# Kernel optimization log

Measured on AMD Instinct MI355X. Metric: run time of the kernel, lower is better.

The kernel has to match this reference:

```python
import jax, jax.numpy as jnp
import numpy as np

N_NODES = 20000
N_EDGES = 320000
F_IN = 512
F_OUT = 1024
N_GRAPHS = 64


def gcn_conv(x, src, dst, ew, W, b, n_nodes):
    xw = x @ W  # [N, Fout]
    loop = jnp.arange(n_nodes)
    s = jnp.concatenate([src, loop])
    d = jnp.concatenate([dst, loop])
    w = jnp.concatenate([ew, jnp.ones((n_nodes,), dtype=x.dtype)])
    deg = jax.ops.segment_sum(w, d, num_segments=n_nodes)  # in-degree by weight
    dinv = jnp.where(deg > 0, jax.lax.rsqrt(deg), 0.0).astype(x.dtype)
    norm = dinv[s] * w * dinv[d]  # [E+N]
    msg = norm[:, None] * xw[s]  # [E+N, Fout]
    out = jax.ops.segment_sum(msg, d, num_segments=n_nodes)
    return out + b


def mean_pool(x, batch, n_graphs):
    sums = jax.ops.segment_sum(x, batch, num_segments=n_graphs)
    cnt = jax.ops.segment_sum(jnp.ones((x.shape[0],), dtype=x.dtype), batch, num_segments=n_graphs)
    return sums / jnp.maximum(cnt, 1.0)[:, None]


def setup_inputs() -> dict:
    key = jax.random.key(0)
    ks = jax.random.split(key, 8)
    node_features = jax.random.normal(ks[0], (N_NODES, F_IN), dtype=jnp.float32)
    edge_index = jax.random.randint(ks[1], (2, N_EDGES), 0, N_NODES, dtype=jnp.int64)
    edge_weight = jax.random.uniform(ks[2], (N_EDGES,), dtype=jnp.float32)
    batch = jnp.sort(jax.random.randint(ks[3], (N_NODES,), 0, N_GRAPHS, dtype=jnp.int64))
    # Glorot-style params for the two GCNConv layers
    W1 = jax.random.normal(ks[4], (F_IN, F_OUT), dtype=jnp.float32) / np.sqrt(F_IN)
    b1 = jnp.zeros((F_OUT,), dtype=jnp.float32)
    W2 = jax.random.normal(ks[5], (F_OUT, F_OUT), dtype=jnp.float32) / np.sqrt(F_OUT)
    b2 = jnp.zeros((F_OUT,), dtype=jnp.float32)
    return {"node_features": node_features, "edge_index": edge_index,
            "edge_weight": edge_weight, "batch": batch,
            "W1": W1, "b1": b1, "W2": W2, "b2": b2}


def reference(node_features, edge_index, edge_weight, batch, W1, b1, W2, b2):
    n_nodes = node_features.shape[0]
    src, dst = edge_index[0], edge_index[1]
    h = jax.nn.relu(gcn_conv(node_features, src, dst, edge_weight, W1, b1, n_nodes))
    h = jax.nn.relu(gcn_conv(h, src, dst, edge_weight, W2, b2, n_nodes))
    return mean_pool(h, batch, N_GRAPHS)  # [G, F_OUT]
```

## Files before the change

kernel.cpp:

```cpp
#include <hip/hip_runtime.h>

#define N_NODES 20000
#define N_PAD   20480
#define N_EDGES 320000
#define F_IN 512
#define F_OUT 1024
#define N_GRAPHS 64
#define ESTRIDE 64

typedef __attribute__((ext_vector_type(8))) short bf16x8;
typedef __attribute__((ext_vector_type(4))) float f32x4;
typedef __attribute__((ext_vector_type(8))) unsigned short ushort8v;

static __device__ __forceinline__ unsigned short f2bf(float f) {
    unsigned int u = __float_as_uint(f);
    u = (u + 0x7fff + ((u >> 16) & 1)) >> 16;
    return (unsigned short)u;
}
static __device__ __forceinline__ float bf2f(unsigned short s) {
    return __uint_as_float(((unsigned int)s) << 16);
}

__global__ void k_setup(float* deg, int* cursor, float* out,
                        const int* __restrict__ batch, int* gstart) {
    int i = blockIdx.x * 256 + threadIdx.x;
    if (i < N_NODES) { deg[i] = 1.0f; cursor[i] = 0; }
    if (i < N_GRAPHS * F_OUT) out[i] = 0.f;
    if (i <= N_GRAPHS) {
        if (i == N_GRAPHS) gstart[i] = N_NODES;
        else {
            int lo = 0, hi = N_NODES;
            while (lo < hi) {
                int mid = (lo + hi) >> 1;
                if (batch[mid] < i) lo = mid + 1; else hi = mid;
            }
            gstart[i] = lo;
        }
    }
}

#define NB_E    ((N_EDGES + 255) / 256)
#define NB_WT   ((F_OUT / 32) * (F_IN / 32 + F_OUT / 32))
#define NB_CX   (N_PAD * (F_IN / 8) / 256)
__global__ __launch_bounds__(256) void k_pre(const int* __restrict__ dst,
                                             const float* __restrict__ ew,
                                             float* deg,
                                             const float* __restrict__ W1,
                                             unsigned short* __restrict__ Wt1,
                                             const float* __restrict__ W2,
                                             unsigned short* __restrict__ Wt2,
                                             const float* __restrict__ x,
                                             unsigned short* __restrict__ xb) {
    __shared__ float tile[32][33];
    const int bid = blockIdx.x;
    if (bid < NB_E) {
        int e = bid * 256 + threadIdx.x;
        if (e < N_EDGES) atomicAdd(&deg[dst[e]], ew[e]);
    } else if (bid < NB_E + NB_WT) {
        int cid = bid - NB_E;
        int by = cid >> 5;
        int n0 = (cid & 31) * 32;
        const float* W; unsigned short* Wt; int K, k0;
        if (by < F_IN / 32) { W = W1; Wt = Wt1; K = F_IN;  k0 = by * 32; }
        else                { W = W2; Wt = Wt2; K = F_OUT; k0 = (by - F_IN / 32) * 32; }
        int tx = threadIdx.x & 31;
        int ty = threadIdx.x >> 5;
#pragma unroll
        for (int i = 0; i < 32; i += 8)
            tile[ty + i][tx] = W[(size_t)(k0 + ty + i) * F_OUT + n0 + tx];
        __syncthreads();
#pragma unroll
        for (int i = 0; i < 32; i += 8)
            Wt[(size_t)(n0 + ty + i) * K + k0 + tx] = f2bf(tile[tx][ty + i]);
    } else {
        int idx = (bid - NB_E - NB_WT) * 256 + threadIdx.x;
        int row = idx >> 6;
        int c8 = (idx & 63) * 8;
        if (row >= N_PAD) return;
        ushort8v v;
        if (row < N_NODES) {
            const float* p = &x[(size_t)row * F_IN + c8];
#pragma unroll
            for (int i = 0; i < 8; i++) v[i] = f2bf(p[i]);
        } else {
#pragma unroll
            for (int i = 0; i < 8; i++) v[i] = 0;
        }
        *(ushort8v*)&xb[(size_t)row * F_IN + c8] = v;
    }
}

__global__ void k_fill(const int* __restrict__ src, const int* __restrict__ dst,
                       const float* __restrict__ ew, const float* __restrict__ deg,
                       int* cursor, unsigned int* __restrict__ csre) {
    int e = blockIdx.x * 256 + threadIdx.x;
    if (e < N_EDGES) {
        int d = dst[e], s = src[e];
        int pos = atomicAdd(&cursor[d], 1);
        if (pos < ESTRIDE) {
            float w = rsqrtf(deg[s]) * ew[e] * rsqrtf(deg[d]);
            csre[d * ESTRIDE + pos] = ((unsigned int)f2bf(w) << 16) | (unsigned int)s;
        }
    }
}

__global__ __launch_bounds__(64) void k_aggr_slab(const unsigned short* __restrict__ xin,
                                                  const float* __restrict__ deg,
                                                  const int* __restrict__ cursor,
                                                  const unsigned int* __restrict__ csre,
                                                  const float* __restrict__ bias,
                                                  unsigned short* __restrict__ outp,
                                                  int F, int act) {
    const int bid = blockIdx.x;
    const int slab = bid & 7;
    const int ng = bid >> 3;
    const int lane = threadIdx.x;
    const int n = ng * 8 + (lane >> 3);
    const int c = blockIdx.y * 512 + slab * 64 + (lane & 7) * 8;

    if (n >= N_NODES) {
        ushort8v z;
#pragma unroll
        for (int i = 0; i < 8; i++) z[i] = 0;
        *(ushort8v*)&outp[(size_t)n * F + c] = z;
        return;
    }

    const float di = rsqrtf(deg[n]);
    const float wself = di * di;
    float a[8];
    {
        ushort8v v = *(const ushort8v*)&xin[(size_t)n * F + c];
#pragma unroll
        for (int i = 0; i < 8; i++) a[i] = bf2f(v[i]) * wself;
    }

    const unsigned int* ce = csre + (size_t)n * ESTRIDE;
    const int cnt = min(cursor[n], ESTRIDE);
    int j = 0;
    for (; j + 4 <= cnt; j += 4) {
        uint4 m = *(const uint4*)&ce[j];
        ushort8v u0 = *(const ushort8v*)&xin[(size_t)(m.x & 0xFFFF) * F + c];
        ushort8v u1 = *(const ushort8v*)&xin[(size_t)(m.y & 0xFFFF) * F + c];
        ushort8v u2 = *(const ushort8v*)&xin[(size_t)(m.z & 0xFFFF) * F + c];
        ushort8v u3 = *(const ushort8v*)&xin[(size_t)(m.w & 0xFFFF) * F + c];
        float w0 = bf2f((unsigned short)(m.x >> 16));
        float w1 = bf2f((unsigned short)(m.y >> 16));
        float w2 = bf2f((unsigned short)(m.z >> 16));
        float w3 = bf2f((unsigned short)(m.w >> 16));
#pragma unroll
        for (int i = 0; i < 8; i++) {
            a[i] += w0 * bf2f(u0[i]);
            a[i] += w1 * bf2f(u1[i]);
            a[i] += w2 * bf2f(u2[i]);
            a[i] += w3 * bf2f(u3[i]);
        }
    }
    for (; j < cnt; j++) {
        unsigned int m = ce[j];
        float w = bf2f((unsigned short)(m >> 16));
        ushort8v u = *(const ushort8v*)&xin[(size_t)(m & 0xFFFF) * F + c];
#pragma unroll
        for (int i = 0; i < 8; i++) a[i] += w * bf2f(u[i]);
    }

    ushort8v r;
    if (act) {
#pragma unroll
        for (int i = 0; i < 8; i++) r[i] = f2bf(fmaxf(a[i] + bias[c + i], 0.f));
    } else {
#pragma unroll
        for (int i = 0; i < 8; i++) r[i] = f2bf(a[i]);
    }
    *(ushort8v*)&outp[(size_t)n * F + c] = r;
}

__global__ __launch_bounds__(512) void k_gemm_ring3(const unsigned short* __restrict__ A,
                                                    const unsigned short* __restrict__ Bt,
                                                    unsigned short* __restrict__ C, int K,
                                                    const float* __restrict__ bias, int act) {
    __shared__ short As[3][128 * 64];
    __shared__ short Bs[3][256 * 64];

    const int bid = blockIdx.x;
    const int xcd = bid & 7;
    const int i2 = bid >> 3;
    const int colb = i2 & 3;
    const int rowb = xcd * 20 + (i2 >> 2);
    const int row0 = rowb * 128;
    const int col0 = colb * 256;

    const int tid = threadIdx.x;
    const int lane = tid & 63;
    const int wave = tid >> 6;
    const int wm = wave >> 2;
    const int wn = wave & 3;
    const int l16 = lane & 15;
    const int kq = lane >> 4;

    const int NT = K >> 6;

    f32x4 acc[4][4] = {};

    auto stage = [&](int t, int s) {
        const int k0 = t * 64;
#pragma unroll
        for (int it = 0; it < 2; it++) {
            int q = it * 512 + tid;
            int r = q >> 3;
            int g = (q & 7) ^ (r & 7);
            __builtin_amdgcn_global_load_lds(
                (const __attribute__((address_space(1))) void*)&A[(size_t)(row0 + r) * K + k0 + g * 8],
                (__attribute__((address_space(3))) void*)&As[s][q * 8], 16, 0, 0);
        }
#pragma unroll
        for (int it = 0; it < 4; it++) {
            int q = it * 512 + tid;
            int r = q >> 3;
            int g = (q & 7) ^ (r & 7);
            __builtin_amdgcn_global_load_lds(
                (const __attribute__((address_space(1))) void*)&Bt[(size_t)(col0 + r) * K + k0 + g * 8],
                (__attribute__((address_space(3))) void*)&Bs[s][q * 8], 16, 0, 0);
        }
    };

    stage(0, 0);
    stage(1, 1);
    asm volatile("s_waitcnt vmcnt(6)" ::: "memory");
    __builtin_amdgcn_s_barrier();
    __builtin_amdgcn_sched_barrier(0);

    int s = 0;
    for (int t = 0; t < NT; ++t) {
        int s2 = s + 2; if (s2 >= 3) s2 -= 3;
        if (t + 2 < NT) stage(t + 2, s2);

        const short* Asl = As[s];
        const short* Bsl = Bs[s];
#pragma unroll
        for (int ks = 0; ks < 2; ks++) {
            bf16x8 af[4], bfr[4];
#pragma unroll
            for (int fr = 0; fr < 4; fr++) {
                int r = wm * 64 + fr * 16 + l16;
                int g = (ks * 4 + kq) ^ (r & 7);
                af[fr] = *(const bf16x8*)&Asl[r * 64 + g * 8];
            }
#pragma unroll
            for (int fc = 0; fc < 4; fc++) {
                int r = wn * 64 + fc * 16 + l16;
                int g = (ks * 4 + kq) ^ (r & 7);
                bfr[fc] = *(const bf16x8*)&Bsl[r * 64 + g * 8];
            }
            __builtin_amdgcn_s_setprio(1);
#pragma unroll
            for (int fr = 0; fr < 4; fr++)
#pragma unroll
                for (int fc = 0; fc < 4; fc++)
                    acc[fr][fc] = __builtin_amdgcn_mfma_f32_16x16x32_bf16(
                        af[fr], bfr[fc], acc[fr][fc], 0, 0, 0);
            __builtin_amdgcn_s_setprio(0);
        }

        if (t < NT - 1) {
            if (t + 2 < NT) asm volatile("s_waitcnt vmcnt(6)" ::: "memory");
            else            asm volatile("s_waitcnt vmcnt(0)" ::: "memory");
            __builtin_amdgcn_s_barrier();
            __builtin_amdgcn_sched_barrier(0);
        }
        s = s + 1; if (s >= 3) s -= 3;
    }

#pragma unroll
    for (int fr = 0; fr < 4; fr++) {
        int m0 = row0 + wm * 64 + fr * 16 + kq * 4;
#pragma unroll
        for (int fc = 0; fc < 4; fc++) {
            int n = col0 + wn * 64 + fc * 16 + l16;
            float bv = act ? bias[n] : 0.f;
#pragma unroll
            for (int reg = 0; reg < 4; reg++) {
                float v = acc[fr][fc][reg];
                if (act) v = fmaxf(v + bv, 0.f);
                C[(size_t)(m0 + reg) * F_OUT + n] = f2bf(v);
            }
        }
    }
}

__global__ __launch_bounds__(256) void k_pool(const unsigned short* __restrict__ h,
                                              const int* __restrict__ batch,
                                              const int* __restrict__ gstart,
                                              float* __restrict__ out) {
    const int r0 = blockIdx.x * 64;
    const int rowsub = threadIdx.x >> 7;
    const int c = (threadIdx.x & 127) * 8;
    const int rend = min(r0 + 64, N_NODES);
    int row = r0 + rowsub;
    if (row >= rend) return;

    float a[8] = {};
    int gcur = batch[row];
    for (; row < rend; row += 2) {
        int g = batch[row];
        if (g != gcur) {
            float inv = 1.0f / (float)max(gstart[gcur + 1] - gstart[gcur], 1);
#pragma unroll
            for (int i = 0; i < 8; i++) {
                atomicAdd(&out[(size_t)gcur * F_OUT + c + i], a[i] * inv);
                a[i] = 0.f;
            }
            gcur = g;
        }
        ushort8v v = *(const ushort8v*)&h[(size_t)row * F_OUT + c];
#pragma unroll
        for (int i = 0; i < 8; i++) a[i] += bf2f(v[i]);
    }
    float inv = 1.0f / (float)max(gstart[gcur + 1] - gstart[gcur], 1);
#pragma unroll
    for (int i = 0; i < 8; i++)
        atomicAdd(&out[(size_t)gcur * F_OUT + c + i], a[i] * inv);
}

extern "C" void kernel_launch(void* const* d_in, const int* in_sizes, int n_in,
                              void* d_out, int out_size, void* d_ws, size_t ws_size,
                              hipStream_t stream) {
    const float* x    = (const float*)d_in[0];
    const int* ei     = (const int*)d_in[1];
    const float* ew   = (const float*)d_in[2];
    const int* batch  = (const int*)d_in[3];
    const float* W1   = (const float*)d_in[4];
    const float* b1   = (const float*)d_in[5];
    const float* W2   = (const float*)d_in[6];
    const float* b2   = (const float*)d_in[7];
    float* out = (float*)d_out;

    const int* src = ei;
    const int* dst = ei + N_EDGES;

    char* ws = (char*)d_ws;
    const size_t SZ_XB  = (size_t)N_PAD * F_IN * 2;
    const size_t SZ_AX  = (size_t)N_PAD * F_IN * 2;
    const size_t SZ_WT1 = (size_t)F_OUT * F_IN * 2;
    const size_t SZ_WT2 = (size_t)F_OUT * F_OUT * 2;
    const size_t SZ_B   = (size_t)N_PAD * F_OUT * 2;
    unsigned short* xb  = (unsigned short*)(ws);
    unsigned short* ax  = (unsigned short*)(ws + SZ_XB);
    unsigned short* Wt1 = (unsigned short*)(ws + SZ_XB + SZ_AX);
    unsigned short* Wt2 = (unsigned short*)(ws + SZ_XB + SZ_AX + SZ_WT1);
    unsigned short* h1  = (unsigned short*)(ws + SZ_XB + SZ_AX + SZ_WT1 + SZ_WT2);
    unsigned short* xw2 = (unsigned short*)(ws + SZ_XB + SZ_AX + SZ_WT1 + SZ_WT2 + SZ_B);
    unsigned short* h2  = (unsigned short*)(ws);
    size_t off = SZ_XB + SZ_AX + SZ_WT1 + SZ_WT2 + 2 * SZ_B;
    auto alloc = [&](size_t bytes) -> void* {
        void* p = ws + off;
        off += (bytes + 255) & ~(size_t)255;
        return p;
    };
    float*        deg    = (float*)       alloc((size_t)N_NODES * 4);
    int*          cursor = (int*)         alloc((size_t)N_NODES * 4);
    unsigned int* csre   = (unsigned int*)alloc((size_t)N_NODES * ESTRIDE * 4);
    int*          gstart = (int*)         alloc((size_t)(N_GRAPHS + 1) * 4);

    k_setup<<<(N_GRAPHS * F_OUT + 255) / 256, 256, 0, stream>>>(deg, cursor, out, batch, gstart);
    k_pre<<<NB_E + NB_WT + NB_CX, 256, 0, stream>>>(dst, ew, deg, W1, Wt1, W2, Wt2, x, xb);
    k_fill<<<NB_E, 256, 0, stream>>>(src, dst, ew, deg, cursor, csre);
    k_aggr_slab<<<dim3((N_PAD / 8) * 8, 1), 64, 0, stream>>>(xb, deg, cursor, csre,
                                                             (const float*)nullptr, ax, F_IN, 0);
    const int gemm_blocks = (N_PAD / 128) * (F_OUT / 256);
    k_gemm_ring3<<<gemm_blocks, 512, 0, stream>>>(ax, Wt1, h1, F_IN, b1, 1);
    k_gemm_ring3<<<gemm_blocks, 512, 0, stream>>>(h1, Wt2, xw2, F_OUT, (const float*)nullptr, 0);
    k_aggr_slab<<<dim3((N_PAD / 8) * 8, 2), 64, 0, stream>>>(xw2, deg, cursor, csre, b2, h2, F_OUT, 1);
    k_pool<<<(N_NODES + 63) / 64, 256, 0, stream>>>(h2, batch, gstart, out);
}
```

Baseline: 375.0 us.

## Fuse mean-pool into second aggregation and switch GEMM to double-buffered 128x128 tiles

```diff
diff --git a/kernel.cpp b/kernel.cpp
--- a/kernel.cpp
+++ b/kernel.cpp
@@ -110,7 +110,10 @@
                                                   const unsigned int* __restrict__ csre,
                                                   const float* __restrict__ bias,
                                                   unsigned short* __restrict__ outp,
-                                                  int F, int act) {
+                                                  int F, int act,
+                                                  const int* __restrict__ batch,
+                                                  const int* __restrict__ gstart,
+                                                  float* __restrict__ pool_out) {
     const int bid = blockIdx.x;
     const int slab = bid & 7;
     const int ng = bid >> 3;
@@ -119,10 +122,12 @@
     const int c = blockIdx.y * 512 + slab * 64 + (lane & 7) * 8;
 
     if (n >= N_NODES) {
-        ushort8v z;
-#pragma unroll
-        for (int i = 0; i < 8; i++) z[i] = 0;
-        *(ushort8v*)&outp[(size_t)n * F + c] = z;
+        if (!pool_out) {
+            ushort8v z;
+#pragma unroll
+            for (int i = 0; i < 8; i++) z[i] = 0;
+            *(ushort8v*)&outp[(size_t)n * F + c] = z;
+        }
         return;
     }
 
@@ -164,6 +169,33 @@
         for (int i = 0; i < 8; i++) a[i] += w * bf2f(u[i]);
     }
 
+    if (pool_out) {
+        float v[8];
+#pragma unroll
+        for (int i = 0; i < 8; i++) v[i] = fmaxf(a[i] + bias[c + i], 0.f);
+        const int g0 = batch[ng * 8];
+        const int g7 = batch[ng * 8 + 7];
+        if (g0 == g7) {
+            const float inv = 1.0f / (float)max(gstart[g0 + 1] - gstart[g0], 1);
+#pragma unroll
+            for (int m = 8; m < 64; m <<= 1)
+#pragma unroll
+                for (int i = 0; i < 8; i++) v[i] += __shfl_xor(v[i], m, 64);
+            if ((lane >> 3) == 0) {
+#pragma unroll
+                for (int i = 0; i < 8; i++)
+                    atomicAdd(&pool_out[(size_t)g0 * F_OUT + c + i], v[i] * inv);
+            }
+        } else {
+            const int g = batch[n];
+            const float inv = 1.0f / (float)max(gstart[g + 1] - gstart[g], 1);
+#pragma unroll
+            for (int i = 0; i < 8; i++)
+                atomicAdd(&pool_out[(size_t)g * F_OUT + c + i], v[i] * inv);
+        }
+        return;
+    }
+
     ushort8v r;
     if (act) {
 #pragma unroll
@@ -175,49 +207,40 @@
     *(ushort8v*)&outp[(size_t)n * F + c] = r;
 }
 
-__global__ __launch_bounds__(512) void k_gemm_ring3(const unsigned short* __restrict__ A,
-                                                    const unsigned short* __restrict__ Bt,
-                                                    unsigned short* __restrict__ C, int K,
-                                                    const float* __restrict__ bias, int act) {
-    __shared__ short As[3][128 * 64];
-    __shared__ short Bs[3][256 * 64];
-
+__global__ __launch_bounds__(256) void k_gemm_db(const unsigned short* __restrict__ A,
+                                                 const unsigned short* __restrict__ Bt,
+                                                 unsigned short* __restrict__ C, int K,
+                                                 const float* __restrict__ bias, int act) {
+    __shared__ short As[2][128 * 64];
+    __shared__ short Bs[2][128 * 64];
     const int bid = blockIdx.x;
     const int xcd = bid & 7;
     const int i2 = bid >> 3;
-    const int colb = i2 & 3;
-    const int rowb = xcd * 20 + (i2 >> 2);
+    const int colb = i2 & 7;
+    const int rowb = xcd * 20 + (i2 >> 3);
     const int row0 = rowb * 128;
-    const int col0 = colb * 256;
+    const int col0 = colb * 128;
 
     const int tid = threadIdx.x;
     const int lane = tid & 63;
     const int wave = tid >> 6;
-    const int wm = wave >> 2;
-    const int wn = wave & 3;
+    const int wm = wave >> 1, wn = wave & 1;
     const int l16 = lane & 15;
     const int kq = lane >> 4;
 
     const int NT = K >> 6;
-
     f32x4 acc[4][4] = {};
 
     auto stage = [&](int t, int s) {
         const int k0 = t * 64;
 #pragma unroll
-        for (int it = 0; it < 2; it++) {
-            int q = it * 512 + tid;
+        for (int it = 0; it < 4; it++) {
+            int q = it * 256 + tid;
             int r = q >> 3;
             int g = (q & 7) ^ (r & 7);
             __builtin_amdgcn_global_load_lds(
                 (const __attribute__((address_space(1))) void*)&A[(size_t)(row0 + r) * K + k0 + g * 8],
                 (__attribute__((address_space(3))) void*)&As[s][q * 8], 16, 0, 0);
-        }
-#pragma unroll
-        for (int it = 0; it < 4; it++) {
-            int q = it * 512 + tid;
-            int r = q >> 3;
-            int g = (q & 7) ^ (r & 7);
             __builtin_amdgcn_global_load_lds(
                 (const __attribute__((address_space(1))) void*)&Bt[(size_t)(col0 + r) * K + k0 + g * 8],
                 (__attribute__((address_space(3))) void*)&Bs[s][q * 8], 16, 0, 0);
@@ -225,16 +248,14 @@
     };
 
     stage(0, 0);
-    stage(1, 1);
-    asm volatile("s_waitcnt vmcnt(6)" ::: "memory");
-    __builtin_amdgcn_s_barrier();
-    __builtin_amdgcn_sched_barrier(0);
+    __syncthreads();
 
     int s = 0;
     for (int t = 0; t < NT; ++t) {
-        int s2 = s + 2; if (s2 >= 3) s2 -= 3;
-        if (t + 2 < NT) stage(t + 2, s2);
-
+        if (t + 1 < NT) {
+            stage(t + 1, s ^ 1);
+            __builtin_amdgcn_sched_barrier(0);
+        }
         const short* Asl = As[s];
         const short* Bsl = Bs[s];
 #pragma unroll
@@ -261,14 +282,10 @@
                         af[fr], bfr[fc], acc[fr][fc], 0, 0, 0);
             __builtin_amdgcn_s_setprio(0);
         }
-
-        if (t < NT - 1) {
-            if (t + 2 < NT) asm volatile("s_waitcnt vmcnt(6)" ::: "memory");
-            else            asm volatile("s_waitcnt vmcnt(0)" ::: "memory");
-            __builtin_amdgcn_s_barrier();
-            __builtin_amdgcn_sched_barrier(0);
-        }
-        s = s + 1; if (s >= 3) s -= 3;
+        if (t + 1 < NT) {
+            __syncthreads();
+            s ^= 1;
+        }
     }
 
 #pragma unroll
@@ -286,40 +303,6 @@
             }
         }
     }
-}
-
-__global__ __launch_bounds__(256) void k_pool(const unsigned short* __restrict__ h,
-                                              const int* __restrict__ batch,
-                                              const int* __restrict__ gstart,
-                                              float* __restrict__ out) {
-    const int r0 = blockIdx.x * 64;
-    const int rowsub = threadIdx.x >> 7;
-    const int c = (threadIdx.x & 127) * 8;
-    const int rend = min(r0 + 64, N_NODES);
-    int row = r0 + rowsub;
-    if (row >= rend) return;
-
-    float a[8] = {};
-    int gcur = batch[row];
-    for (; row < rend; row += 2) {
-        int g = batch[row];
-        if (g != gcur) {
-            float inv = 1.0f / (float)max(gstart[gcur + 1] - gstart[gcur], 1);
-#pragma unroll
-            for (int i = 0; i < 8; i++) {
-                atomicAdd(&out[(size_t)gcur * F_OUT + c + i], a[i] * inv);
-                a[i] = 0.f;
-            }
-            gcur = g;
-        }
-        ushort8v v = *(const ushort8v*)&h[(size_t)row * F_OUT + c];
-#pragma unroll
-        for (int i = 0; i < 8; i++) a[i] += bf2f(v[i]);
-    }
-    float inv = 1.0f / (float)max(gstart[gcur + 1] - gstart[gcur], 1);
-#pragma unroll
-    for (int i = 0; i < 8; i++)
-        atomicAdd(&out[(size_t)gcur * F_OUT + c + i], a[i] * inv);
 }
 
 extern "C" void kernel_launch(void* const* d_in, const int* in_sizes, int n_in,
@@ -350,7 +333,6 @@
     unsigned short* Wt2 = (unsigned short*)(ws + SZ_XB + SZ_AX + SZ_WT1);
     unsigned short* h1  = (unsigned short*)(ws + SZ_XB + SZ_AX + SZ_WT1 + SZ_WT2);
     unsigned short* xw2 = (unsigned short*)(ws + SZ_XB + SZ_AX + SZ_WT1 + SZ_WT2 + SZ_B);
-    unsigned short* h2  = (unsigned short*)(ws);
     size_t off = SZ_XB + SZ_AX + SZ_WT1 + SZ_WT2 + 2 * SZ_B;
     auto alloc = [&](size_t bytes) -> void* {
         void* p = ws + off;
@@ -366,10 +348,12 @@
     k_pre<<<NB_E + NB_WT + NB_CX, 256, 0, stream>>>(dst, ew, deg, W1, Wt1, W2, Wt2, x, xb);
     k_fill<<<NB_E, 256, 0, stream>>>(src, dst, ew, deg, cursor, csre);
     k_aggr_slab<<<dim3((N_PAD / 8) * 8, 1), 64, 0, stream>>>(xb, deg, cursor, csre,
-                                                             (const float*)nullptr, ax, F_IN, 0);
-    const int gemm_blocks = (N_PAD / 128) * (F_OUT / 256);
-    k_gemm_ring3<<<gemm_blocks, 512, 0, stream>>>(ax, Wt1, h1, F_IN, b1, 1);
-    k_gemm_ring3<<<gemm_blocks, 512, 0, stream>>>(h1, Wt2, xw2, F_OUT, (const float*)nullptr, 0);
-    k_aggr_slab<<<dim3((N_PAD / 8) * 8, 2), 64, 0, stream>>>(xw2, deg, cursor, csre, b2, h2, F_OUT, 1);
-    k_pool<<<(N_NODES + 63) / 64, 256, 0, stream>>>(h2, batch, gstart, out);
-}
+                                                             (const float*)nullptr, ax, F_IN, 0,
+                                                             batch, gstart, (float*)nullptr);
+    const int gemm_blocks = (N_PAD / 128) * (F_OUT / 128);
+    k_gemm_db<<<gemm_blocks, 256, 0, stream>>>(ax, Wt1, h1, F_IN, b1, 1);
+    k_gemm_db<<<gemm_blocks, 256, 0, stream>>>(h1, Wt2, xw2, F_OUT, (const float*)nullptr, 0);
+    k_aggr_slab<<<dim3((N_PAD / 8) * 8, 2), 64, 0, stream>>>(xw2, deg, cursor, csre, b2,
+                                                             (unsigned short*)nullptr, F_OUT, 1,
+                                                             batch, gstart, out);
+}
```

Result: slower. 494.8 us (+32.0%).
